# Optimization experiments

Measured on AMD Instinct MI355X. Metric: run time of the kernel, lower is better.

## Reference

```python
import jax, jax.numpy as jnp
import numpy as np

B = 2
D = 256
NH = 8
DH = D // NH
L = 4
K = 2                       # sampling grid per box side
NP = K * K                  # sampled points per level
FF = 1024
NQ = 300
NE = 6
ND = 6
REF_SIZE = 4.0
SHAPES = ((64, 64), (32, 32), (16, 16), (8, 8))
S = sum(h * w for h, w in SHAPES)


def make_ref_windows():
    ws = []
    for (H, W) in SHAPES:
        y = (jnp.arange(1, H + 1, dtype=jnp.float32) - 0.5) / (H + 1e-6)
        x = (jnp.arange(1, W + 1, dtype=jnp.float32) - 0.5) / (W + 1e-6)
        yy, xx = jnp.meshgrid(y, x, indexing='ij')
        ctr = jnp.stack([xx, yy], -1).reshape(-1, 2)
        size = jnp.broadcast_to(jnp.array([REF_SIZE / W, REF_SIZE / H], jnp.float32), ctr.shape)
        ws.append(jnp.concatenate([ctr, size], -1))
    return jnp.broadcast_to(jnp.concatenate(ws, 0)[None], (B, S, 4))


def layernorm(x, g, b):
    m = jnp.mean(x, -1, keepdims=True)
    v = jnp.mean((x - m) ** 2, -1, keepdims=True)
    return (x - m) / jnp.sqrt(v + 1e-5) * g + b


def inverse_sigmoid(x, eps=1e-5):
    x = jnp.clip(x, eps, 1.0 - eps)
    return jnp.log(x / (1.0 - x))


def bilinear_sample(vl, pts, Hl, Wl):
    # vl: [B, Hl*Wl, NH, DH], pts: [B, N, NP, 2] normalized to [0,1]
    x = pts[..., 0] * Wl - 0.5
    y = pts[..., 1] * Hl - 0.5
    x0f = jnp.floor(x); y0f = jnp.floor(y)
    wx = x - x0f; wy = y - y0f
    x0 = x0f.astype(jnp.int32); y0 = y0f.astype(jnp.int32)
    Bn, N, P = x.shape

    def gather(yi, xi):
        valid = ((xi >= 0) & (xi < Wl) & (yi >= 0) & (yi < Hl)).astype(vl.dtype)
        idx = jnp.clip(yi, 0, Hl - 1) * Wl + jnp.clip(xi, 0, Wl - 1)
        g = jnp.take_along_axis(vl, idx.reshape(Bn, N * P, 1, 1), axis=1)
        return g.reshape(Bn, N, P, NH, DH) * valid[..., None, None]

    w00 = ((1 - wx) * (1 - wy))[..., None, None]
    w01 = (wx * (1 - wy))[..., None, None]
    w10 = ((1 - wx) * wy)[..., None, None]
    w11 = (wx * wy)[..., None, None]
    return (gather(y0, x0) * w00 + gather(y0, x0 + 1) * w01
            + gather(y0 + 1, x0) * w10 + gather(y0 + 1, x0 + 1) * w11)


def box_attention(q, memory, ref_windows, Wv, bv, Wa, ba, Wo, bo):
    # q: [B,N,D], memory: [B,S,D], ref_windows: [B,N,4] (cx,cy,w,h)
    Bn, N, _ = q.shape
    v = (memory @ Wv + bv).reshape(Bn, memory.shape[1], NH, DH)
    attn = jax.nn.softmax((q @ Wa + ba).reshape(Bn, N, NH, L * NP), axis=-1)
    g = (jnp.arange(K, dtype=jnp.float32) + 0.5) / K - 0.5   # grid fractions in box
    gy, gx = jnp.meshgrid(g, g, indexing='ij')
    grid = jnp.stack([gx.ravel(), gy.ravel()], -1)           # [NP,2]
    pts = ref_windows[:, :, None, :2] + grid[None, None] * ref_windows[:, :, None, 2:]
    out = jnp.zeros((Bn, N, NH, DH), q.dtype)
    start = 0
    for l, (Hl, Wl) in enumerate(SHAPES):
        sl = Hl * Wl
        sampled = bilinear_sample(v[:, start:start + sl], pts, Hl, Wl)  # [B,N,NP,NH,DH]
        out = out + jnp.einsum('bnphd,bnhp->bnhd', sampled, attn[..., l * NP:(l + 1) * NP])
        start += sl
    return out.reshape(Bn, N, D) @ Wo + bo


def mha(q_in, k_in, v_in, Wqkv, bqkv, Wo, bo):
    Bn, N, _ = q_in.shape
    q = (q_in @ Wqkv[:, :D] + bqkv[:D]).reshape(Bn, N, NH, DH)
    k = (k_in @ Wqkv[:, D:2 * D] + bqkv[D:2 * D]).reshape(Bn, N, NH, DH)
    v = (v_in @ Wqkv[:, 2 * D:] + bqkv[2 * D:]).reshape(Bn, N, NH, DH)
    a = jax.nn.softmax(jnp.einsum('bqhd,bkhd->bhqk', q, k) / jnp.sqrt(jnp.float32(DH)), axis=-1)
    o = jnp.einsum('bhqk,bkhd->bqhd', a, v).reshape(Bn, N, D)
    return o @ Wo + bo


def pos_embed_2d(coords):
    # coords: [B,N,2] -> [B,N,D] sine embedding (deformable-DETR style)
    npf = D // 2
    dim_t = 10000.0 ** (2.0 * (jnp.arange(npf) // 2) / npf)
    p = coords[..., None] * (2 * np.pi) / dim_t               # [B,N,2,npf]
    p = jnp.stack([jnp.sin(p[..., 0::2]), jnp.cos(p[..., 1::2])], -1)
    return p.reshape(coords.shape[0], coords.shape[1], 2 * npf)


def reference(src, pos, eWv, ebv, eWa, eba, eWo, ebo, eW1, eb1, eW2, eb2,
              en1g, en1b, en2g, en2b,
              dWqkv, dbqkv, dWso, dbso, dWv, dbv, dWa, dba, dWo, dbo,
              dW1, db1, dW2, db2, dn1g, dn1b, dn2g, dn2b, dn3g, dn3b,
              cls_w, cls_b, bb_w1, bb_b1, bb_w2, bb_b2, bb_w3, bb_b3,
              el_w, el_b, el_g, el_beta):
    ref_windows = make_ref_windows()
    out = src
    for i in range(NE):
        a = box_attention(out + pos, out, ref_windows, eWv[i], ebv[i], eWa[i], eba[i], eWo[i], ebo[i])
        out = layernorm(out + a, en1g[i], en1b[i])
        f = jax.nn.relu(out @ eW1[i] + eb1[i]) @ eW2[i] + eb2[i]
        out = layernorm(out + f, en2g[i], en2b[i])
    # proposal selection (topk + gather)
    valid = jnp.all((ref_windows[..., :2] > 0.01) & (ref_windows[..., :2] < 0.99), axis=-1)
    logits = (out @ cls_w + cls_b)[..., 0]
    logits = jnp.where(valid, logits, -65504.0)
    _, idx = jax.lax.top_k(logits, NQ)
    q_emb = jnp.take_along_axis(out, idx[..., None], axis=1)
    tgt = layernorm(jax.lax.stop_gradient(q_emb) @ el_w + el_b, el_g, el_beta)
    ref_sel = jnp.take_along_axis(ref_windows, idx[..., None], axis=1)
    h = jax.nn.relu(q_emb @ bb_w1 + bb_b1)
    h = jax.nn.relu(h @ bb_w2 + bb_b2)
    tmp = h @ bb_w3 + bb_b3 + inverse_sigmoid(ref_sel)
    out_ref = jax.lax.stop_gradient(jax.nn.sigmoid(tmp))
    query_pos = pos_embed_2d(out_ref[..., :2]) + pos_embed_2d(out_ref[..., 2:])
    # decoder
    x = tgt
    inter = []
    for i in range(ND):
        qk = x + query_pos
        sa = mha(qk, qk, x, dWqkv[i], dbqkv[i], dWso[i], dbso[i])
        x = layernorm(x + sa, dn1g[i], dn1b[i])
        ca = box_attention(x + query_pos, out, out_ref, dWv[i], dbv[i], dWa[i], dba[i], dWo[i], dbo[i])
        x = layernorm(x + ca, dn2g[i], dn2b[i])
        f = jax.nn.relu(x @ dW1[i] + db1[i]) @ dW2[i] + db2[i]
        x = layernorm(x + f, dn3g[i], dn3b[i])
        inter.append(x)
    return jnp.stack(inter)  # [ND, B, NQ, D]


def setup_inputs() -> dict:
    key = jax.random.key(0)
    kit = iter(jax.random.split(key, 80))
    def rn(shape, s=0.02):
        return jax.random.normal(next(kit), shape, jnp.float32) * s
    z = lambda *sh: jnp.zeros(sh, jnp.float32)
    o = lambda *sh: jnp.ones(sh, jnp.float32)
    A = NH * L * NP
    return dict(
        src=jax.random.normal(next(kit), (B, S, D), jnp.float32),
        pos=jax.random.normal(next(kit), (B, S, D), jnp.float32),
        eWv=rn((NE, D, D)), ebv=z(NE, D), eWa=rn((NE, D, A)), eba=z(NE, A),
        eWo=rn((NE, D, D)), ebo=z(NE, D),
        eW1=rn((NE, D, FF)), eb1=z(NE, FF), eW2=rn((NE, FF, D)), eb2=z(NE, D),
        en1g=o(NE, D), en1b=z(NE, D), en2g=o(NE, D), en2b=z(NE, D),
        dWqkv=rn((ND, D, 3 * D)), dbqkv=z(ND, 3 * D),
        dWso=rn((ND, D, D)), dbso=z(ND, D),
        dWv=rn((ND, D, D)), dbv=z(ND, D), dWa=rn((ND, D, A)), dba=z(ND, A),
        dWo=rn((ND, D, D)), dbo=z(ND, D),
        dW1=rn((ND, D, FF)), db1=z(ND, FF), dW2=rn((ND, FF, D)), db2=z(ND, D),
        dn1g=o(ND, D), dn1b=z(ND, D), dn2g=o(ND, D), dn2b=z(ND, D), dn3g=o(ND, D), dn3b=z(ND, D),
        cls_w=rn((D, 1)), cls_b=z(1),
        bb_w1=rn((D, D)), bb_b1=z(D), bb_w2=rn((D, D)), bb_b2=z(D),
        bb_w3=rn((D, 4)), bb_b3=z(4),
        el_w=rn((D, D)), el_b=z(D), el_g=o(D), el_beta=z(D),
    )
```

## Files before the change

### kernel.cpp

```cpp
#include <hip/hip_runtime.h>
#include <hip/hip_bf16.h>
#include <math.h>

typedef unsigned short u16;
typedef unsigned int u32;
typedef unsigned long long u64;

#define Bc   2
#define NHc  8
#define Sc   5440
#define NQc  300
#define NEc  6
#define NDc  6
#define FFc  1024
#define BSc  (Bc*Sc)
#define BNQc (Bc*NQc)

__device__ __forceinline__ float us2f(u16 u) {
    union { float f; unsigned v; } x; x.v = ((unsigned)u) << 16; return x.f;
}

__device__ __forceinline__ u16 f2bf(float f) {
    unsigned u = __float_as_uint(f);
    unsigned r = u + 0x7FFFu + ((u >> 16) & 1u);
    return (u16)(r >> 16);
}
__device__ __forceinline__ float bf2f(u16 u) { return us2f(u); }
__device__ __forceinline__ unsigned pk2(u16 a, u16 b) { return (unsigned)a | ((unsigned)b << 16); }

using bf16x8 = __attribute__((ext_vector_type(8))) short;
using f32x4  = __attribute__((ext_vector_type(4))) float;

__global__ void k_detect(const u16* __restrict__ src, int* __restrict__ flag) {
    __shared__ int cnt;
    if (threadIdx.x == 0) cnt = 0;
    __syncthreads();
    u16 v = src[threadIdx.x];
    int e = (v >> 7) & 0xFF;
    int plaus = (e == 0) || (e >= 107 && e <= 131);
    atomicAdd(&cnt, plaus);
    __syncthreads();
    if (threadIdx.x == 0) *flag = (cnt >= 224) ? 1 : 0;
}

struct CvtArgs {
    const void* in[48];
    long off[48];
    int n[48];
    int cnt;
    long total;
};
__global__ void k_cvt_all8(CvtArgs args, float* __restrict__ out,
                           const int* __restrict__ flag) {
    long g = ((long)blockIdx.x * 256 + threadIdx.x) * 8;
    if (g >= args.total) return;
    int lo = 0, hi = args.cnt - 1;
    while (lo < hi) {
        int mid = (lo + hi + 1) >> 1;
        if (args.off[mid] <= g) lo = mid; else hi = mid - 1;
    }
    long local = g - args.off[lo];
    long n = (long)args.n[lo];
    float v[8];
#pragma unroll
    for (int j = 0; j < 8; ++j) v[j] = 0.f;
    if (*flag) {
        const u16* p = (const u16*)args.in[lo] + local;
        if (local + 8 <= n) {
            uint4 r = *(const uint4*)p;
            const u16* pu = (const u16*)&r;
#pragma unroll
            for (int j = 0; j < 8; ++j) v[j] = us2f(pu[j]);
        } else {
            for (int j = 0; j < 8; ++j)
                if (local + j < n) v[j] = us2f(p[j]);
        }
    } else {
        const float* p = (const float*)args.in[lo] + local;
        if (local + 8 <= n) {
            float4 a = ((const float4*)p)[0];
            float4 b = ((const float4*)p)[1];
            v[0] = a.x; v[1] = a.y; v[2] = a.z; v[3] = a.w;
            v[4] = b.x; v[5] = b.y; v[6] = b.z; v[7] = b.w;
        } else {
            for (int j = 0; j < 8; ++j)
                if (local + j < n) v[j] = p[j];
        }
    }
    float4 o0, o1;
    o0.x = v[0]; o0.y = v[1]; o0.z = v[2]; o0.w = v[3];
    o1.x = v[4]; o1.y = v[5]; o1.z = v[6]; o1.w = v[7];
    ((float4*)(out + g))[0] = o0;
    ((float4*)(out + g))[1] = o1;
}

__global__ void k_addf(const float* __restrict__ a, const float* __restrict__ b,
                       float* __restrict__ o,
                       u16* __restrict__ oh, u16* __restrict__ ol, int n) {
    int i = blockIdx.x * 256 + threadIdx.x;
    if (i >= n) return;
    float s = a[i] + (b ? b[i] : 0.f);
    if (o) o[i] = s;
    if (oh) {
        u16 h = f2bf(s);
        oh[i] = h;
        ol[i] = f2bf(s - bf2f(h));
    }
}

template<int RELU>
__global__ __launch_bounds__(256) void k_mgemm(
    const u16* __restrict__ Ah, const u16* __restrict__ Al,
    const float* __restrict__ W, const u16* __restrict__ Wraw, int ldw,
    const float* __restrict__ bias,
    float* __restrict__ C, u16* __restrict__ Ch, u16* __restrict__ Cl,
    int ldc, int K,
    const int* __restrict__ flag) {
    __shared__ __align__(16) u16 lsAH[4096];
    __shared__ __align__(16) u16 lsAL[4096];
    __shared__ __align__(16) u16 lsBH[4096];
    __shared__ __align__(16) u16 lsBL[4096];
    const int t = threadIdx.x;
    const int row0 = blockIdx.y * 128, col0 = blockIdx.x * 128;
    const int fast = *flag;

    const int c0 = t, c1 = 256 + t;
    const u16* a0h = Ah + (size_t)(row0 + (c0 & 127)) * K + (c0 >> 7) * 8;
    const u16* a1h = Ah + (size_t)(row0 + (c1 & 127)) * K + (c1 >> 7) * 8;
    const u16* a0l = Al + (size_t)(row0 + (c0 & 127)) * K + (c0 >> 7) * 8;
    const u16* a1l = Al + (size_t)(row0 + (c1 & 127)) * K + (c1 >> 7) * 8;

    const int bkp = t >> 4, bno = t & 15;
    const float* bp = W + (size_t)(bkp * 2) * ldw + col0 + bno * 8;
    const u16*  brp = Wraw + (size_t)(bkp * 2) * ldw + col0 + bno * 8;

    const int lane = t & 63;
    const int w = t >> 6;
    const int wr = (w >> 1) * 64, wc = (w & 1) * 64;
    const int kg = lane >> 4, lr = lane & 15;

    f32x4 acc[4][4] = {};
    uint4 aU0h, aU1h, aU0l, aU1l;
    float4 bR[4];
    uint4 bU0, bU1;
    aU0h = *(const uint4*)a0h;
    aU1h = *(const uint4*)a1h;
    aU0l = *(const uint4*)a0l;
    aU1l = *(const uint4*)a1l;
    if (fast) {
        bU0 = *(const uint4*)brp;
        bU1 = *(const uint4*)(brp + ldw);
    } else {
        const float4* q0 = (const float4*)bp;
        const float4* q1 = (const float4*)(bp + ldw);
        bR[0] = q0[0]; bR[1] = q0[1]; bR[2] = q1[0]; bR[3] = q1[1];
    }

    for (int k0 = 0; k0 < K; k0 += 32) {
        if (k0) __syncthreads();
        *(uint4*)&lsAH[(unsigned)c0 * 8u] = aU0h;
        *(uint4*)&lsAH[(unsigned)c1 * 8u] = aU1h;
        *(uint4*)&lsAL[(unsigned)c0 * 8u] = aU0l;
        *(uint4*)&lsAL[(unsigned)c1 * 8u] = aU1l;
        {
            unsigned bb = (unsigned)(bkp >> 2) * 1024u + (unsigned)(bkp & 3) * 2u;
            if (fast) {
                const u16* e0 = (const u16*)&bU0;
                const u16* e1 = (const u16*)&bU1;
#pragma unroll
                for (int j = 0; j < 8; ++j) {
                    int slot = bno * 8 + (j ^ (bno & 7));
                    *(unsigned*)&lsBH[bb + (unsigned)slot * 8u] = pk2(e0[j], e1[j]);
                }
            } else {
                float e0f[8], e1f[8];
                *(float4*)&e0f[0] = bR[0]; *(float4*)&e0f[4] = bR[1];
                *(float4*)&e1f[0] = bR[2]; *(float4*)&e1f[4] = bR[3];
#pragma unroll
                for (int j = 0; j < 8; ++j) {
                    int slot = bno * 8 + (j ^ (bno & 7));
                    u16 h0 = f2bf(e0f[j]), h1 = f2bf(e1f[j]);
                    *(unsigned*)&lsBH[bb + (unsigned)slot * 8u] = pk2(h0, h1);
                    u16 l0 = f2bf(e0f[j] - bf2f(h0));
                    u16 l1 = f2bf(e1f[j] - bf2f(h1));
                    *(unsigned*)&lsBL[bb + (unsigned)slot * 8u] = pk2(l0, l1);
                }
            }
        }
        __syncthreads();
        if (k0 + 32 < K) {
            aU0h = *(const uint4*)(a0h + k0 + 32);
            aU1h = *(const uint4*)(a1h + k0 + 32);
            aU0l = *(const uint4*)(a0l + k0 + 32);
            aU1l = *(const uint4*)(a1l + k0 + 32);
            if (fast) {
                bU0 = *(const uint4*)(brp + (size_t)(k0 + 32) * ldw);
                bU1 = *(const uint4*)(brp + (size_t)(k0 + 33) * ldw);
            } else {
                const float4* q0 = (const float4*)(bp + (size_t)(k0 + 32) * ldw);
                const float4* q1 = (const float4*)(bp + (size_t)(k0 + 33) * ldw);
                bR[0] = q0[0]; bR[1] = q0[1]; bR[2] = q1[0]; bR[3] = q1[1];
            }
        }
        bf16x8 aH[4], aL[4], bH[4], bL[4];
#pragma unroll
        for (int mi = 0; mi < 4; ++mi) {
            unsigned ia = (unsigned)kg * 1024u + (unsigned)(wr + mi * 16 + lr) * 8u;
            aH[mi] = *(const bf16x8*)&lsAH[ia];
            aL[mi] = *(const bf16x8*)&lsAL[ia];
        }
#pragma unroll
        for (int ni = 0; ni < 4; ++ni) {
            int c = wc + ni * 16 + lr;
            int slot = (c & ~7) | ((c ^ (c >> 3)) & 7);
            unsigned ib = (unsigned)kg * 1024u + (unsigned)slot * 8u;
            bH[ni] = *(const bf16x8*)&lsBH[ib];
            if (!fast) bL[ni] = *(const bf16x8*)&lsBL[ib];
        }
#pragma unroll
        for (int mi = 0; mi < 4; ++mi)
#pragma unroll
            for (int ni = 0; ni < 4; ++ni) {
                acc[mi][ni] = __builtin_amdgcn_mfma_f32_16x16x32_bf16(aH[mi], bH[ni], acc[mi][ni], 0, 0, 0);
                acc[mi][ni] = __builtin_amdgcn_mfma_f32_16x16x32_bf16(aL[mi], bH[ni], acc[mi][ni], 0, 0, 0);
            }
        if (!fast) {
#pragma unroll
            for (int mi = 0; mi < 4; ++mi)
#pragma unroll
                for (int ni = 0; ni < 4; ++ni)
                    acc[mi][ni] = __builtin_amdgcn_mfma_f32_16x16x32_bf16(aH[mi], bL[ni], acc[mi][ni], 0, 0, 0);
        }
    }
    const int rb = row0 + wr + (lane >> 4) * 4;
#pragma unroll
    for (int ni = 0; ni < 4; ++ni) {
        int cc = col0 + wc + ni * 16 + lr;
        float bv = bias[cc];
#pragma unroll
        for (int mi = 0; mi < 4; ++mi) {
#pragma unroll
            for (int r2 = 0; r2 < 4; ++r2) {
                int rr = rb + mi * 16 + r2;
                float v = acc[mi][ni][r2] + bv;
                if (RELU) v = fmaxf(v, 0.f);
                size_t ox = (size_t)rr * ldc + cc;
                if (C) C[ox] = v;
                if (Ch) {
                    u16 h = f2bf(v);
                    Ch[ox] = h;
                    Cl[ox] = f2bf(v - bf2f(h));
                }
            }
        }
    }
}

template<int RELU>
__global__ __launch_bounds__(256) void k_dgemm(
    const float* __restrict__ A, int lda,
    const float* __restrict__ W, int ldw, int wcol0,
    const float* __restrict__ bias,
    float* __restrict__ C, int ldc,
    int M, int N, int K) {
    __shared__ float As[2][16][68];
    __shared__ float Bs[2][16][68];
    int t = threadIdx.x;
    int row0 = blockIdx.y * 64, col0 = blockIdx.x * 64;
    int ti = t >> 4, tj = t & 15;
    int arow = t >> 2, akq = (t & 3) << 2;
    int bk = t >> 4, bn = (t & 15) << 2;
    bool aok = (row0 + arow) < M;
    const float* ap = A + (size_t)(row0 + arow) * lda + akq;
    const float* bp = W + (size_t)bk * ldw + wcol0 + col0 + bn;
    float4 aR = aok ? *(const float4*)ap : make_float4(0.f, 0.f, 0.f, 0.f);
    float4 bR = *(const float4*)bp;
    As[0][akq + 0][arow] = aR.x;
    As[0][akq + 1][arow] = aR.y;
    As[0][akq + 2][arow] = aR.z;
    As[0][akq + 3][arow] = aR.w;
    *(float4*)&Bs[0][bk][bn] = bR;
    __syncthreads();
    int cur = 0;
    float acc[4][4] = {};
    for (int k0 = 0; k0 < K; k0 += 16) {
        bool more = (k0 + 16) < K;
        if (more) {
            aR = aok ? *(const float4*)(ap + k0 + 16) : make_float4(0.f, 0.f, 0.f, 0.f);
            bR = *(const float4*)(bp + (size_t)(k0 + 16) * ldw);
        }
#pragma unroll
        for (int k = 0; k < 16; ++k) {
            float a[4], b[4];
#pragma unroll
            for (int r = 0; r < 4; ++r) a[r] = As[cur][k][ti * 4 + r];
#pragma unroll
            for (int c = 0; c < 4; ++c) b[c] = Bs[cur][k][tj * 4 + c];
#pragma unroll
            for (int r = 0; r < 4; ++r)
#pragma unroll
                for (int c = 0; c < 4; ++c) acc[r][c] += a[r] * b[c];
        }
        if (more) {
            int nxt = cur ^ 1;
            As[nxt][akq + 0][arow] = aR.x;
            As[nxt][akq + 1][arow] = aR.y;
            As[nxt][akq + 2][arow] = aR.z;
            As[nxt][akq + 3][arow] = aR.w;
            *(float4*)&Bs[nxt][bk][bn] = bR;
            __syncthreads();
            cur = nxt;
        }
    }
    for (int r = 0; r < 4; ++r) {
        int rr = row0 + ti * 4 + r;
        if (rr >= M) continue;
        for (int c = 0; c < 4; ++c) {
            int cc = col0 + tj * 4 + c;
            float v = acc[r][c] + bias[cc];
            if (RELU) v = fmaxf(v, 0.f);
            C[(size_t)rr * ldc + cc] = v;
        }
    }
}

__global__ __launch_bounds__(256) void k_gemm4(
    const float* __restrict__ A, const float* __restrict__ W,
    const float* __restrict__ bias, const float* __restrict__ rsel,
    float* __restrict__ oref, int M, int K) {
    int row = blockIdx.x * 64 + (threadIdx.x >> 2);
    int col = threadIdx.x & 3;
    if (row >= M) return;
    float acc = 0.f;
    const float* a = A + (size_t)row * K;
    for (int k = 0; k < K; ++k) acc += a[k] * W[k * 4 + col];
    float tmp = acc + bias[col];
    float r = rsel[(size_t)row * 4 + col];
    r = fminf(fmaxf(r, 1e-5f), 1.f - 1e-5f);
    float v = tmp + logf(r / (1.f - r));
    oref[(size_t)row * 4 + col] = 1.f / (1.f + __expf(-v));
}

__global__ void k_ln(const float* __restrict__ a, const float* __restrict__ b,
                     const float* __restrict__ g, const float* __restrict__ be,
                     float* __restrict__ o,
                     u16* __restrict__ oh, u16* __restrict__ ol,
                     const float* __restrict__ padd, float* __restrict__ opadd,
                     u16* __restrict__ oph, u16* __restrict__ opl,
                     void* __restrict__ sdst, size_t soff,
                     const int* __restrict__ flag) {
    int row = blockIdx.x;
    int t = threadIdx.x;
    __shared__ float red[256];
    size_t ix = (size_t)row * 256 + t;
    float x = a[ix];
    if (b) x += b[ix];
    red[t] = x;
    __syncthreads();
    for (int s = 128; s > 0; s >>= 1) { if (t < s) red[t] += red[t + s]; __syncthreads(); }
    float mean = red[0] / 256.f;
    __syncthreads();
    float d = x - mean;
    red[t] = d * d;
    __syncthreads();
    for (int s = 128; s > 0; s >>= 1) { if (t < s) red[t] += red[t + s]; __syncthreads(); }
    float var = red[0] / 256.f;
    float y = d * rsqrtf(var + 1e-5f) * g[t] + be[t];
    o[ix] = y;
    if (oh) {
        u16 h = f2bf(y);
        oh[ix] = h;
        ol[ix] = f2bf(y - bf2f(h));
    }
    if (padd) {
        float z = y + padd[ix];
        if (opadd) opadd[ix] = z;
        if (oph) {
            u16 h = f2bf(z);
            oph[ix] = h;
            opl[ix] = f2bf(z - bf2f(h));
        }
    }
    if (sdst) {
        if (*flag) ((__hip_bfloat16*)sdst)[soff + ix] = __float2bfloat16(y);
        else       ((float*)sdst)[soff + ix] = y;
    }
}

__global__ void k_refw(float* __restrict__ rw) {
    int s = blockIdx.x * 256 + threadIdx.x;
    if (s >= Sc) return;
    int start, HW;
    if (s < 4096)      { start = 0;    HW = 64; }
    else if (s < 5120) { start = 4096; HW = 32; }
    else if (s < 5376) { start = 5120; HW = 16; }
    else               { start = 5376; HW = 8;  }
    int loc = s - start;
    int i = loc / HW, j = loc % HW;
    rw[s * 4 + 0] = (j + 0.5f) / ((float)HW + 1e-6f);
    rw[s * 4 + 1] = (i + 0.5f) / ((float)HW + 1e-6f);
    rw[s * 4 + 2] = 4.0f / (float)HW;
    rw[s * 4 + 3] = 4.0f / (float)HW;
}

__global__ __launch_bounds__(256) void k_box_sample4(
    const float* __restrict__ v, const float* __restrict__ attn,
    const float* __restrict__ refw, int ref_bs,
    float* __restrict__ out, u16* __restrict__ outh, u16* __restrict__ outl,
    int N) {
    const int t = threadIdx.x;
    const int qi = t >> 6, lane = t & 63;
    const int n = blockIdx.x * 4 + qi;
    const int b = blockIdx.y;
    if (n >= N) return;
    const float* arow = attn + ((size_t)b * N + n) * 128;
    float2 wl = *(const float2*)(arow + lane * 2);
    float m = fmaxf(wl.x, wl.y);
#pragma unroll
    for (int d2 = 1; d2 < 8; d2 <<= 1) m = fmaxf(m, __shfl_xor(m, d2, 8));
    float e0 = __expf(wl.x - m), e1 = __expf(wl.y - m);
    float s = e0 + e1;
#pragma unroll
    for (int d2 = 1; d2 < 8; d2 <<= 1) s += __shfl_xor(s, d2, 8);
    float inv = 1.f / s;
    e0 *= inv; e1 *= inv;

    const float* rw = refw + (size_t)ref_bs * b + (size_t)n * 4;
    float cx = rw[0], cy = rw[1], bw = rw[2], bh = rw[3];
    const float* vb = v + (size_t)b * Sc * 256 + lane * 4;
    float4 acc = make_float4(0.f, 0.f, 0.f, 0.f);
    int start = 0;
    const int HWs[4] = {64, 32, 16, 8};
#pragma unroll
    for (int l = 0; l < 4; ++l) {
        int HW = HWs[l];
#pragma unroll
        for (int p = 0; p < 4; ++p) {
            float gx = (p & 1) ? 0.25f : -0.25f;
            float gy = (p >> 1) ? 0.25f : -0.25f;
            float x = (cx + gx * bw) * (float)HW - 0.5f;
            float y = (cy + gy * bh) * (float)HW - 0.5f;
            float x0f = floorf(x), y0f = floorf(y);
            float wx = x - x0f, wy = y - y0f;
            int x0 = (int)x0f, y0 = (int)y0f;
            float4 smp = make_float4(0.f, 0.f, 0.f, 0.f);
            if (x0 >= 0 && x0 < HW && y0 >= 0 && y0 < HW) {
                float4 g4 = *(const float4*)(vb + (size_t)(start + y0 * HW + x0) * 256);
                float wgt = (1.f - wx) * (1.f - wy);
                smp.x += wgt * g4.x; smp.y += wgt * g4.y; smp.z += wgt * g4.z; smp.w += wgt * g4.w;
            }
            if (x0 + 1 >= 0 && x0 + 1 < HW && y0 >= 0 && y0 < HW) {
                float4 g4 = *(const float4*)(vb + (size_t)(start + y0 * HW + x0 + 1) * 256);
                float wgt = wx * (1.f - wy);
                smp.x += wgt * g4.x; smp.y += wgt * g4.y; smp.z += wgt * g4.z; smp.w += wgt * g4.w;
            }
            if (x0 >= 0 && x0 < HW && y0 + 1 >= 0 && y0 + 1 < HW) {
                float4 g4 = *(const float4*)(vb + (size_t)(start + (y0 + 1) * HW + x0) * 256);
                float wgt = (1.f - wx) * wy;
                smp.x += wgt * g4.x; smp.y += wgt * g4.y; smp.z += wgt * g4.z; smp.w += wgt * g4.w;
            }
            if (x0 + 1 >= 0 && x0 + 1 < HW && y0 + 1 >= 0 && y0 + 1 < HW) {
                float4 g4 = *(const float4*)(vb + (size_t)(start + (y0 + 1) * HW + x0 + 1) * 256);
                float wgt = wx * wy;
                smp.x += wgt * g4.x; smp.y += wgt * g4.y; smp.z += wgt * g4.z; smp.w += wgt * g4.w;
            }
            const int idx = l * 4 + p;
            float wsel = (idx & 1) ? e1 : e0;
            float wv = __shfl(wsel, (lane & ~7) | (idx >> 1), 64);
            acc.x += wv * smp.x; acc.y += wv * smp.y;
            acc.z += wv * smp.z; acc.w += wv * smp.w;
        }
        start += HW * HW;
    }
    size_t obase = ((size_t)b * N + n) * 256 + lane * 4;
    if (out) *(float4*)(out + obase) = acc;
    if (outh) {
        ushort4 h, lo;
        h.x = f2bf(acc.x); h.y = f2bf(acc.y); h.z = f2bf(acc.z); h.w = f2bf(acc.w);
        lo.x = f2bf(acc.x - bf2f(h.x)); lo.y = f2bf(acc.y - bf2f(h.y));
        lo.z = f2bf(acc.z - bf2f(h.z)); lo.w = f2bf(acc.w - bf2f(h.w));
        *(ushort4*)(outh + obase) = h;
        *(ushort4*)(outl + obase) = lo;
    }
}

__global__ void k_cls(const float* __restrict__ x, const float* __restrict__ w,
                      const float* __restrict__ cb, const float* __restrict__ rw,
                      float* __restrict__ logits) {
    int row = blockIdx.x;
    int t = threadIdx.x;
    __shared__ float red[256];
    red[t] = x[(size_t)row * 256 + t] * w[t];
    __syncthreads();
    for (int s = 128; s > 0; s >>= 1) { if (t < s) red[t] += red[t + s]; __syncthreads(); }
    if (t == 0) {
        int s = row % Sc;
        float cx = rw[s * 4], cy = rw[s * 4 + 1];
        bool valid = (cx > 0.01f) && (cx < 0.99f) && (cy > 0.01f) && (cy < 0.99f);
        logits[row] = valid ? (red[0] + cb[0]) : -65504.0f;
    }
}

__global__ void k_topk(const float* __restrict__ logits, int* __restrict__ idxout) {
    int b = blockIdx.x;
    int t = threadIdx.x;
    __shared__ unsigned keys[Sc];
    __shared__ int hist[256];
    __shared__ unsigned sprefix;
    __shared__ int sR;
    __shared__ int cnt;
    __shared__ u64 cand[512];
    for (int i = t; i < Sc; i += 256) {
        union { float f; unsigned u; } x;
        x.f = logits[(size_t)b * Sc + i];
        unsigned u = x.u;
        keys[i] = (u & 0x80000000u) ? ~u : (u | 0x80000000u);
    }
    if (t == 0) { sprefix = 0; sR = NQc; }
    __syncthreads();
    for (int shift = 24; shift >= 0; shift -= 8) {
        hist[t] = 0;
        __syncthreads();
        unsigned pref = sprefix;
        unsigned pmask = (shift == 24) ? 0u : (0xFFFFFFFFu << (shift + 8));
        for (int i = t; i < Sc; i += 256) {
            unsigned kk = keys[i];
            if ((kk & pmask) == (pref & pmask))
                atomicAdd(&hist[(kk >> shift) & 255], 1);
        }
        __syncthreads();
        if (t == 0) {
            int R = sR, cum = 0;
            for (int bin = 255; bin >= 0; --bin) {
                cum += hist[bin];
                if (cum >= R) {
                    sR = R - (cum - hist[bin]);
                    sprefix = pref | ((unsigned)bin << shift);
                    break;
                }
            }
        }
        __syncthreads();
    }
    unsigned T = sprefix;
    if (t == 0) cnt = 0;
    __syncthreads();
    for (int i = t; i < Sc; i += 256) {
        unsigned kk = keys[i];
        if (kk >= T) {
            int slot = atomicAdd(&cnt, 1);
            if (slot < 512)
                cand[slot] = ~((((u64)kk) << 32) | (u64)(0xFFFFFFFFu - (unsigned)i));
        }
    }
    __syncthreads();
    int total = cnt < 512 ? cnt : 512;
    for (int i = t; i < 512; i += 256)
        if (i >= total) cand[i] = 0xFFFFFFFFFFFFFFFFull;
    __syncthreads();
    for (int k = 2; k <= 512; k <<= 1) {
        for (int j = k >> 1; j > 0; j >>= 1) {
#pragma unroll
            for (int bb = 0; bb < 2; ++bb) {
                int i = t + bb * 256;
                int ixj = i ^ j;
                if (ixj > i) {
                    bool up = ((i & k) == 0);
                    u64 a = cand[i], c = cand[ixj];
                    if (up ? (a > c) : (a < c)) { cand[i] = c; cand[ixj] = a; }
                }
            }
            __syncthreads();
        }
    }
    for (int s = t; s < NQc; s += 256) {
        u64 c = ~cand[s];
        idxout[b * NQc + s] = (int)(0xFFFFFFFFu - (unsigned)(c & 0xFFFFFFFFull));
    }
}

__global__ void k_gather(const float* __restrict__ x, const float* __restrict__ rw,
                         const int* __restrict__ idx, float* __restrict__ qemb,
                         float* __restrict__ refsel) {
    int q = blockIdx.x, b = blockIdx.y;
    int t = threadIdx.x;
    int id = idx[b * NQc + q];
    qemb[((size_t)b * NQc + q) * 256 + t] = x[((size_t)b * Sc + id) * 256 + t];
    if (t < 4) refsel[((size_t)b * NQc + q) * 4 + t] = rw[id * 4 + t];
}

__global__ void k_qpos(const float* __restrict__ outref, float* __restrict__ qpos) {
    int n = blockIdx.x, b = blockIdx.y;
    int t = threadIdx.x;
    const float* orf = outref + ((size_t)b * NQc + n) * 4;
    int c = t >> 7;
    int j = (t & 127) >> 1;
    int si = t & 1;
    float tj = powf(10000.f, (float)j / 64.f);
    float sc = 6.283185307179586f / tj;
    float v1 = orf[c] * sc;
    float v2 = orf[2 + c] * sc;
    float r = si ? (cosf(v1) + cosf(v2)) : (sinf(v1) + sinf(v2));
    qpos[((size_t)b * NQc + n) * 256 + t] = r;
}

#define NSPL 10
#define SPLW 30
__global__ __launch_bounds__(256) void k_mha2(
    const float* __restrict__ qk, const float* __restrict__ v,
    float* __restrict__ opart, float* __restrict__ mlpart) {
    __shared__ float lsK[SPLW][256];
    __shared__ float lsV[SPLW][256];
    const int t = threadIdx.x;
    const int h = t >> 5, ql = t & 31;
    const int b = blockIdx.y, z = blockIdx.z;
    const int n = blockIdx.x * 32 + ql;
    const bool qok = n < NQc;
    const int kstart = z * SPLW;
    for (int f = t; f < SPLW * 64; f += 256) {
        int r = f >> 6, c4 = f & 63;
        int krow = kstart + r;
        float4 kv = *(const float4*)(qk + (size_t)(b * NQc + krow) * 512 + 256 + c4 * 4);
        float4 vv = *(const float4*)(v + (size_t)(b * NQc + krow) * 256 + c4 * 4);
        *(float4*)&lsK[r][c4 * 4] = kv;
        *(float4*)&lsV[r][c4 * 4] = vv;
    }
    __syncthreads();
    float q[32];
    {
        const float* qp = qk + (size_t)(b * NQc + (qok ? n : 0)) * 512 + h * 32;
#pragma unroll
        for (int j4 = 0; j4 < 8; ++j4) {
            float4 f = ((const float4*)qp)[j4];
            q[j4 * 4 + 0] = f.x; q[j4 * 4 + 1] = f.y;
            q[j4 * 4 + 2] = f.z; q[j4 * 4 + 3] = f.w;
        }
    }
    const float scale = 0.17677669529663688f;
    float s[SPLW];
#pragma unroll
    for (int kk = 0; kk < SPLW; ++kk) {
        float acc = 0.f;
        const float* kr = &lsK[kk][h * 32];
#pragma unroll
        for (int j4 = 0; j4 < 8; ++j4) {
            float4 kf = ((const float4*)kr)[j4];
            acc += q[j4*4+0]*kf.x + q[j4*4+1]*kf.y + q[j4*4+2]*kf.z + q[j4*4+3]*kf.w;
        }
        s[kk] = acc * scale;
    }
    float m = s[0];
#pragma unroll
    for (int kk = 1; kk < SPLW; ++kk) m = fmaxf(m, s[kk]);
    float o[32];
#pragma unroll
    for (int j = 0; j < 32; ++j) o[j] = 0.f;
    float l = 0.f;
#pragma unroll
    for (int kk = 0; kk < SPLW; ++kk) {
        float e = __expf(s[kk] - m);
        l += e;
        const float* vr = &lsV[kk][h * 32];
#pragma unroll
        for (int j4 = 0; j4 < 8; ++j4) {
            float4 vf = ((const float4*)vr)[j4];
            o[j4*4+0] += e * vf.x; o[j4*4+1] += e * vf.y;
            o[j4*4+2] += e * vf.z; o[j4*4+3] += e * vf.w;
        }
    }
    if (qok) {
        float* op = opart + ((size_t)z * BNQc + (size_t)b * NQc + n) * 256 + h * 32;
#pragma unroll
        for (int j4 = 0; j4 < 8; ++j4) {
            float4 f;
            f.x = o[j4*4+0]; f.y = o[j4*4+1]; f.z = o[j4*4+2]; f.w = o[j4*4+3];
            ((float4*)op)[j4] = f;
        }
        float* mlp = mlpart + ((size_t)z * BNQc + (size_t)b * NQc + n) * 16 + h * 2;
        mlp[0] = m; mlp[1] = l;
    }
}

__global__ void k_mha_comb(const float* __restrict__ opart, const float* __restrict__ mlpart,
                           float* __restrict__ out) {
    int row = blockIdx.x;
    int t = threadIdx.x;
    int h = t >> 5;
    float mm[NSPL], ll[NSPL];
    float M = -3.0e38f;
#pragma unroll
    for (int z = 0; z < NSPL; ++z) {
        mm[z] = mlpart[((size_t)z * BNQc + row) * 16 + h * 2];
        ll[z] = mlpart[((size_t)z * BNQc + row) * 16 + h * 2 + 1];
        M = fmaxf(M, mm[z]);
    }
    float denom = 0.f, osum = 0.f;
#pragma unroll
    for (int z = 0; z < NSPL; ++z) {
        float a = __expf(mm[z] - M);
        denom += ll[z] * a;
        osum += opart[((size_t)z * BNQc + row) * 256 + t] * a;
    }
    out[(size_t)row * 256 + t] = osum / denom;
}

extern "C" void kernel_launch(void* const* d_in, const int* in_sizes, int n_in,
                              void* d_out, int out_size, void* d_ws, size_t ws_size,
                              hipStream_t stream) {
    char* base = (char*)d_ws;
    size_t off = 0;
    auto allocB = [&](size_t bytes) {
        char* p = base + off;
        off = (off + bytes + 255) & ~(size_t)255;
        return p;
    };
    int* flag = (int*)allocB(16);
    auto allocF = [&](size_t n) { return (float*)allocB(n * 4); };
    auto allocH = [&](size_t n) { return (u16*)allocB(n * 2); };

    k_detect<<<1, 256, 0, stream>>>((const u16*)d_in[0], flag);

    CvtArgs ca;
    long acc = 0;
    int ninp = n_in < 48 ? n_in : 48;
    for (int i = 0; i < 48; ++i) {
        int idx2 = i < ninp ? i : ninp - 1;
        ca.in[i] = d_in[idx2];
        ca.n[i] = (i < ninp) ? in_sizes[i] : 0;
        ca.off[i] = acc;
        acc += ((long)ca.n[i] + 63) & ~63L;
    }
    ca.cnt = 48;
    ca.total = acc;
    float* cvtbase = allocF((size_t)acc);
    k_cvt_all8<<<(int)((acc / 8 + 255) / 256), 256, 0, stream>>>(ca, cvtbase, flag);
    float* F[48];
    for (int i = 0; i < 48; ++i) F[i] = cvtbase + ca.off[i];

    const size_t BSD = (size_t)BSc * 256;
    float* enc    = F[0];
    u16* encH  = allocH(BSD);  u16* encL  = allocH(BSD);
    u16* pbufH = allocH(BSD);  u16* pbufL = allocH(BSD);
    u16* tbufH = allocH(BSD);  u16* tbufL = allocH(BSD);
    u16* ffnhH = allocH((size_t)BSc * FFc);
    u16* ffnhL = allocH((size_t)BSc * FFc);
    float* vbuf   = allocF(BSD);
    float* gout   = allocF(BSD);
    float* attnb  = allocF((size_t)BSc * 128);
    float* refw   = allocF(Sc * 4);
    float* logit  = allocF(BSc);
    int*   idx    = (int*)allocB(BNQc * 4);
    float* qemb   = allocF((size_t)BNQc * 256);
    float* rsel   = allocF(BNQc * 4);
    float* xbuf   = allocF((size_t)BNQc * 256);
    float* qposb  = allocF((size_t)BNQc * 256);
    float* dqk    = allocF((size_t)BNQc * 256);
    float* dqk512 = allocF((size_t)BNQc * 512);
    float* dv     = allocF((size_t)BNQc * 256);
    float* dt1    = allocF((size_t)BNQc * 256);
    float* dt2    = allocF((size_t)BNQc * 256);
    float* datt   = allocF((size_t)BNQc * 128);
    float* dffnh  = allocF((size_t)BNQc * FFc);
    float* h1f    = allocF((size_t)BNQc * 256);
    float* h2f    = allocF((size_t)BNQc * 256);
    float* oref   = allocF(BNQc * 4);
    float* opart  = allocF((size_t)NSPL * BNQc * 256);
    float* mlpart = allocF((size_t)NSPL * BNQc * 16);
    (void)ws_size; (void)out_size;

    auto MG = [&](int relu, const u16* Ah, const u16* Al, int widx, size_t woff, int ldw,
                  const float* bias, float* Cf, u16* Ch, u16* Cl, int ldc, int N, int K) {
        const float* Wf = F[widx] + woff;
        const u16* Wraw = (const u16*)d_in[widx] + woff;
        dim3 g(N / 128, BSc / 128);
        if (relu) k_mgemm<1><<<g, 256, 0, stream>>>(Ah, Al, Wf, Wraw, ldw, bias, Cf, Ch, Cl, ldc, K, flag);
        else      k_mgemm<0><<<g, 256, 0, stream>>>(Ah, Al, Wf, Wraw, ldw, bias, Cf, Ch, Cl, ldc, K, flag);
    };
    auto DG = [&](int relu, const float* A, int lda, const float* W, int ldw, int wcol0,
                  const float* bias, float* C, int ldc, int M, int N, int K) {
        dim3 g(N / 64, (M + 63) / 64);
        if (relu) k_dgemm<1><<<g, 256, 0, stream>>>(A, lda, W, ldw, wcol0, bias, C, ldc, M, N, K);
        else      k_dgemm<0><<<g, 256, 0, stream>>>(A, lda, W, ldw, wcol0, bias, C, ldc, M, N, K);
    };

    const int nBSD = (int)BSD;
    k_refw<<<(Sc + 255) / 256, 256, 0, stream>>>(refw);
    k_addf<<<(nBSD + 255) / 256, 256, 0, stream>>>(enc, nullptr, nullptr, encH, encL, nBSD);
    k_addf<<<(nBSD + 255) / 256, 256, 0, stream>>>(enc, F[1], nullptr, pbufH, pbufL, nBSD);

    for (int i = 0; i < NEc; ++i) {
        MG(0, encH, encL, 2, (size_t)i * 65536, 256, F[3] + i * 256, vbuf, nullptr, nullptr, 256, 256, 256);
        MG(0, pbufH, pbufL, 4, (size_t)i * 32768, 128, F[5] + i * 128, attnb, nullptr, nullptr, 128, 128, 256);
        k_box_sample4<<<dim3((Sc + 3) / 4, Bc), 256, 0, stream>>>(vbuf, attnb, refw, 0,
                                                                  nullptr, tbufH, tbufL, Sc);
        MG(0, tbufH, tbufL, 6, (size_t)i * 65536, 256, F[7] + i * 256, gout, nullptr, nullptr, 256, 256, 256);
        k_ln<<<BSc, 256, 0, stream>>>(enc, gout, F[12] + i * 256, F[13] + i * 256,
                                      enc, encH, encL,
                                      nullptr, nullptr, nullptr, nullptr,
                                      nullptr, 0, flag);
        MG(1, encH, encL, 8, (size_t)i * 262144, 1024, F[9] + i * 1024,
           nullptr, ffnhH, ffnhL, 1024, 1024, 256);
        MG(0, ffnhH, ffnhL, 10, (size_t)i * 262144, 256, F[11] + i * 256,
           gout, nullptr, nullptr, 256, 256, 1024);
        k_ln<<<BSc, 256, 0, stream>>>(enc, gout, F[14] + i * 256, F[15] + i * 256,
                                      enc, encH, encL,
                                      (i < NEc - 1) ? F[1] : nullptr, nullptr,
                                      (i < NEc - 1) ? pbufH : nullptr,
                                      (i < NEc - 1) ? pbufL : nullptr,
                                      nullptr, 0, flag);
    }

    k_cls<<<BSc, 256, 0, stream>>>(enc, F[36], F[37], refw, logit);
    k_topk<<<Bc, 256, 0, stream>>>(logit, idx);
    k_gather<<<dim3(NQc, Bc), 256, 0, stream>>>(enc, refw, idx, qemb, rsel);
    DG(0, qemb, 256, F[44], 256, 0, F[45], dt1, 256, BNQc, 256, 256);
    DG(1, qemb, 256, F[38], 256, 0, F[39], h1f, 256, BNQc, 256, 256);
    DG(1, h1f,  256, F[40], 256, 0, F[41], h2f, 256, BNQc, 256, 256);
    k_gemm4<<<(BNQc + 63) / 64, 256, 0, stream>>>(h2f, F[42], F[43], rsel, oref, BNQc, 256);
    k_qpos<<<dim3(NQc, Bc), 256, 0, stream>>>(oref, qposb);
    k_ln<<<BNQc, 256, 0, stream>>>(dt1, nullptr, F[46], F[47],
                                   xbuf, nullptr, nullptr,
                                   qposb, dqk, nullptr, nullptr,
                                   nullptr, 0, flag);

    const int nXD = BNQc * 256;
    for (int i = 0; i < NDc; ++i) {
        DG(0, dqk,  256, F[16] + (size_t)i * 196608, 768, 0,   F[17] + i * 768,       dqk512, 512, BNQc, 512, 256);
        DG(0, xbuf, 256, F[16] + (size_t)i * 196608, 768, 512, F[17] + i * 768 + 512, dv,     256, BNQc, 256, 256);
        k_mha2<<<dim3((NQc + 31) / 32, Bc, NSPL), 256, 0, stream>>>(dqk512, dv, opart, mlpart);
        k_mha_comb<<<BNQc, 256, 0, stream>>>(opart, mlpart, dt1);
        DG(0, dt1, 256, F[18] + (size_t)i * 65536, 256, 0, F[19] + i * 256, dt2, 256, BNQc, 256, 256);
        k_ln<<<BNQc, 256, 0, stream>>>(xbuf, dt2, F[30] + i * 256, F[31] + i * 256,
                                       xbuf, nullptr, nullptr,
                                       qposb, dqk, nullptr, nullptr,
                                       nullptr, 0, flag);
        MG(0, encH, encL, 20, (size_t)i * 65536, 256, F[21] + i * 256, vbuf, nullptr, nullptr, 256, 256, 256);
        DG(0, dqk, 256, F[22] + (size_t)i * 32768, 128, 0, F[23] + i * 128, datt, 128, BNQc, 128, 256);
        k_box_sample4<<<dim3((NQc + 3) / 4, Bc), 256, 0, stream>>>(vbuf, datt, oref, NQc * 4,
                                                                   dt1, nullptr, nullptr, NQc);
        DG(0, dt1, 256, F[24] + (size_t)i * 65536, 256, 0, F[25] + i * 256, dt2, 256, BNQc, 256, 256);
        k_ln<<<BNQc, 256, 0, stream>>>(xbuf, dt2, F[32] + i * 256, F[33] + i * 256,
                                       xbuf, nullptr, nullptr,
                                       nullptr, nullptr, nullptr, nullptr,
                                       nullptr, 0, flag);
        DG(1, xbuf,  256,  F[26] + (size_t)i * 262144, 1024, 0, F[27] + i * 1024, dffnh, 1024, BNQc, 1024, 256);
        DG(0, dffnh, 1024, F[28] + (size_t)i * 262144, 256,  0, F[29] + i * 256,  dt2,   256,  BNQc, 256, 1024);
        k_ln<<<BNQc, 256, 0, stream>>>(xbuf, dt2, F[34] + i * 256, F[35] + i * 256,
                                       xbuf, nullptr, nullptr,
                                       (i < NDc - 1) ? qposb : nullptr,
                                       (i < NDc - 1) ? dqk : nullptr, nullptr, nullptr,
                                       d_out, (size_t)i * nXD, flag);
    }
}
```

Measured before the change: 2.885 ms.

## Swizzle workgroups across XCDs, parallelize topk scan and sort, fuse input conversion

Remaps workgroup indices so neighbouring tiles in the GEMM and box-sampling kernels land on the same XCD, aiming for better L2 reuse. Replaces the serial single-thread histogram scan in topk with a parallel suffix-sum, and the bitonic sort with a rank-by-counting pass. Merges the two initial conversion kernels into one launch that reads the input once. The rank-counting step does more comparisons per thread, and the swizzle changes the order in which blocks are scheduled.

```diff
diff --git a/kernel.cpp b/kernel.cpp
--- a/kernel.cpp
+++ b/kernel.cpp
@@ -27,6 +27,13 @@
 }
 __device__ __forceinline__ float bf2f(u16 u) { return us2f(u); }
 __device__ __forceinline__ unsigned pk2(u16 a, u16 b) { return (unsigned)a | ((unsigned)b << 16); }
+
+__device__ __forceinline__ int xcd_swz(int orig, int nwg) {
+    int xcd = orig & 7;
+    int q = nwg >> 3, r = nwg & 7;
+    int base = (xcd < r) ? xcd * (q + 1) : r * (q + 1) + (xcd - r) * q;
+    return base + (orig >> 3);
+}
 
 using bf16x8 = __attribute__((ext_vector_type(8))) short;
 using f32x4  = __attribute__((ext_vector_type(4))) float;
@@ -94,18 +101,19 @@
     ((float4*)(out + g))[1] = o1;
 }
 
-__global__ void k_addf(const float* __restrict__ a, const float* __restrict__ b,
-                       float* __restrict__ o,
-                       u16* __restrict__ oh, u16* __restrict__ ol, int n) {
+__global__ void k_addf2(const float* __restrict__ a, const float* __restrict__ pos,
+                        u16* __restrict__ ah, u16* __restrict__ al,
+                        u16* __restrict__ ph, u16* __restrict__ pl, int n) {
     int i = blockIdx.x * 256 + threadIdx.x;
     if (i >= n) return;
-    float s = a[i] + (b ? b[i] : 0.f);
-    if (o) o[i] = s;
-    if (oh) {
-        u16 h = f2bf(s);
-        oh[i] = h;
-        ol[i] = f2bf(s - bf2f(h));
-    }
+    float x = a[i];
+    u16 h = f2bf(x);
+    ah[i] = h;
+    al[i] = f2bf(x - bf2f(h));
+    float s = x + pos[i];
+    u16 h2 = f2bf(s);
+    ph[i] = h2;
+    pl[i] = f2bf(s - bf2f(h2));
 }
 
 template<int RELU>
@@ -121,7 +129,9 @@
     __shared__ __align__(16) u16 lsBH[4096];
     __shared__ __align__(16) u16 lsBL[4096];
     const int t = threadIdx.x;
-    const int row0 = blockIdx.y * 128, col0 = blockIdx.x * 128;
+    int lin = blockIdx.x + gridDim.x * blockIdx.y;
+    lin = xcd_swz(lin, gridDim.x * gridDim.y);
+    const int row0 = (lin / gridDim.x) * 128, col0 = (lin % gridDim.x) * 128;
     const int fast = *flag;
 
     const int c0 = t, c1 = 256 + t;
@@ -410,7 +420,8 @@
     int N) {
     const int t = threadIdx.x;
     const int qi = t >> 6, lane = t & 63;
-    const int n = blockIdx.x * 4 + qi;
+    const int blk = xcd_swz(blockIdx.x, gridDim.x);
+    const int n = blk * 4 + qi;
     const int b = blockIdx.y;
     if (n >= N) return;
     const float* arow = attn + ((size_t)b * N + n) * 128;
@@ -506,6 +517,7 @@
     int t = threadIdx.x;
     __shared__ unsigned keys[Sc];
     __shared__ int hist[256];
+    __shared__ int suf[257];
     __shared__ unsigned sprefix;
     __shared__ int sR;
     __shared__ int cnt;
@@ -516,12 +528,13 @@
         unsigned u = x.u;
         keys[i] = (u & 0x80000000u) ? ~u : (u | 0x80000000u);
     }
-    if (t == 0) { sprefix = 0; sR = NQc; }
+    if (t == 0) { sprefix = 0; sR = NQc; suf[256] = 0; }
     __syncthreads();
     for (int shift = 24; shift >= 0; shift -= 8) {
         hist[t] = 0;
         __syncthreads();
         unsigned pref = sprefix;
+        int R = sR;
         unsigned pmask = (shift == 24) ? 0u : (0xFFFFFFFFu << (shift + 8));
         for (int i = t; i < Sc; i += 256) {
             unsigned kk = keys[i];
@@ -529,16 +542,17 @@
                 atomicAdd(&hist[(kk >> shift) & 255], 1);
         }
         __syncthreads();
-        if (t == 0) {
-            int R = sR, cum = 0;
-            for (int bin = 255; bin >= 0; --bin) {
-                cum += hist[bin];
-                if (cum >= R) {
-                    sR = R - (cum - hist[bin]);
-                    sprefix = pref | ((unsigned)bin << shift);
-                    break;
-                }
-            }
+        suf[t] = hist[t];
+        __syncthreads();
+        for (int s2 = 1; s2 < 256; s2 <<= 1) {
+            int vv = suf[t] + ((t + s2 < 256) ? suf[t + s2] : 0);
+            __syncthreads();
+            suf[t] = vv;
+            __syncthreads();
+        }
+        if (suf[t] >= R && suf[t + 1] < R) {
+            sR = R - suf[t + 1];
+            sprefix = pref | ((unsigned)t << shift);
         }
         __syncthreads();
     }
@@ -558,24 +572,15 @@
     for (int i = t; i < 512; i += 256)
         if (i >= total) cand[i] = 0xFFFFFFFFFFFFFFFFull;
     __syncthreads();
-    for (int k = 2; k <= 512; k <<= 1) {
-        for (int j = k >> 1; j > 0; j >>= 1) {
-#pragma unroll
-            for (int bb = 0; bb < 2; ++bb) {
-                int i = t + bb * 256;
-                int ixj = i ^ j;
-                if (ixj > i) {
-                    bool up = ((i & k) == 0);
-                    u64 a = cand[i], c = cand[ixj];
-                    if (up ? (a > c) : (a < c)) { cand[i] = c; cand[ixj] = a; }
-                }
-            }
-            __syncthreads();
-        }
-    }
-    for (int s = t; s < NQc; s += 256) {
-        u64 c = ~cand[s];
-        idxout[b * NQc + s] = (int)(0xFFFFFFFFu - (unsigned)(c & 0xFFFFFFFFull));
+    for (int i = t; i < 512; i += 256) {
+        if (i >= total) continue;
+        u64 mine = cand[i];
+        int rank = 0;
+        for (int j = 0; j < 512; ++j) rank += (cand[j] < mine) ? 1 : 0;
+        if (rank < NQc) {
+            u64 c = ~mine;
+            idxout[b * NQc + rank] = (int)(0xFFFFFFFFu - (unsigned)(c & 0xFFFFFFFFull));
+        }
     }
 }
 
@@ -785,8 +790,7 @@
 
     const int nBSD = (int)BSD;
     k_refw<<<(Sc + 255) / 256, 256, 0, stream>>>(refw);
-    k_addf<<<(nBSD + 255) / 256, 256, 0, stream>>>(enc, nullptr, nullptr, encH, encL, nBSD);
-    k_addf<<<(nBSD + 255) / 256, 256, 0, stream>>>(enc, F[1], nullptr, pbufH, pbufL, nBSD);
+    k_addf2<<<(nBSD + 255) / 256, 256, 0, stream>>>(enc, F[1], encH, encL, pbufH, pbufL, nBSD);
 
     for (int i = 0; i < NEc; ++i) {
         MG(0, encH, encL, 2, (size_t)i * 65536, 256, F[3] + i * 256, vbuf, nullptr, nullptr, 256, 256, 256);
```

After: 2.808 ms. -2.7%, faster.
